# Performance work log

Hardware: AMD Instinct MI355X
Metric: run time of the kernel (lower is better)

Reference implementation:

```python
import jax, jax.numpy as jnp
import numpy as np
from jax import lax

K = 20
EPS = 1e-5
SLOPE = 0.2


def knn_idx(x, k):
    # x: [B, C, N] -> idx [B, N, k] of nearest neighbors (incl. self)
    inner = jnp.einsum('bcn,bcm->bnm', x, x)
    sq = jnp.sum(x * x, axis=1)                      # [B, N]
    neg_d = -(sq[:, :, None] + sq[:, None, :] - 2.0 * inner)
    _, idx = lax.top_k(neg_d, k)
    return idx


def graph_feature(x, idx):
    # x: [B, C, N], idx: [B, N, k] -> [B, 2C, N, k]
    B = x.shape[0]
    xt = jnp.transpose(x, (0, 2, 1))                 # [B, N, C]
    neigh = xt[jnp.arange(B)[:, None, None], idx]    # [B, N, k, C]
    center = jnp.broadcast_to(xt[:, :, None, :], neigh.shape)
    feat = jnp.concatenate([neigh - center, center], axis=-1)  # [B, N, k, 2C]
    return jnp.transpose(feat, (0, 3, 1, 2))         # [B, 2C, N, k]


def conv_bn_lrelu(feat, W, gamma, beta):
    # 1x1 Conv2d (no bias) + eval-mode BN (mean=0, var=1) + LeakyReLU(0.2)
    y = jnp.einsum('oc,bcnk->bonk', W, feat)
    scale = gamma / jnp.sqrt(1.0 + EPS)
    y = y * scale[None, :, None, None] + beta[None, :, None, None]
    return jnp.where(y >= 0, y, SLOPE * y)


def setup_inputs() -> dict:
    key = jax.random.key(0)
    ks = jax.random.split(key, 16)
    B, N, emb = 4, 2048, 1024
    d = {'x': jax.random.normal(ks[0], (B, 3, N), dtype=jnp.float32)}
    dims = [(64, 6), (64, 128), (128, 128), (256, 256), (emb, 256)]
    for i, (o, c) in enumerate(dims):
        d[f'W{i+1}'] = jax.random.normal(ks[1 + i], (o, c), dtype=jnp.float32) * (1.0 / np.sqrt(c))
        d[f'g{i+1}'] = 1.0 + 0.1 * jax.random.normal(ks[6 + i], (o,), dtype=jnp.float32)
        d[f'b{i+1}'] = 0.1 * jax.random.normal(ks[11 + i], (o,), dtype=jnp.float32)
    return d


def reference(x, W1, W2, W3, W4, W5, g1, g2, g3, g4, g5, b1, b2, b3, b4, b5):
    # EdgeConv block 1
    f = graph_feature(x, knn_idx(x, K))              # [B, 6, N, k]
    x1 = jnp.max(conv_bn_lrelu(f, W1, g1, b1), axis=-1)   # [B, 64, N]
    # EdgeConv block 2
    f = graph_feature(x1, knn_idx(x1, K))            # [B, 128, N, k]
    x2 = jnp.max(conv_bn_lrelu(f, W2, g2, b2), axis=-1)   # [B, 64, N]
    # EdgeConv block 3
    f = graph_feature(x2, knn_idx(x2, K))            # [B, 128, N, k]
    x3 = jnp.max(conv_bn_lrelu(f, W3, g3, b3), axis=-1)   # [B, 128, N]
    # EdgeConv block 4
    f = graph_feature(x3, knn_idx(x3, K))            # [B, 256, N, k]
    x4 = jnp.max(conv_bn_lrelu(f, W4, g4, b4), axis=-1)   # [B, 256, N]
    # conv5 (1x1 over points) + global max pool
    x5 = conv_bn_lrelu(x4[:, :, :, None], W5, g5, b5)     # [B, emb, N, 1]
    return jnp.max(x5[..., 0], axis=-1)              # [B, emb]
```

## Files before the change

### kernel.cpp

```cpp
#include <hip/hip_runtime.h>
#include <math.h>

#define BB 4
#define NN 2048
#define KK 20
#define INFPK 0xFFFFFFFFFFFFFFFFull

static __device__ __forceinline__ float lrelu(float z) {
    return z >= 0.f ? z : 0.2f * z;
}

template<int CTRL>
static __device__ __forceinline__ unsigned long long dpp_min64_step(unsigned long long v) {
    unsigned lo = (unsigned)__builtin_amdgcn_update_dpp(
        (int)0xFFFFFFFFu, (int)(unsigned)v, CTRL, 0xF, 0xF, false);
    unsigned hi = (unsigned)__builtin_amdgcn_update_dpp(
        (int)0xFFFFFFFFu, (int)(unsigned)(v >> 32), CTRL, 0xF, 0xF, false);
    unsigned long long t = ((unsigned long long)hi << 32) | lo;
    return t < v ? t : v;
}
static __device__ __forceinline__ unsigned long long wave_min64_bcast(unsigned long long v) {
    v = dpp_min64_step<0x111>(v);
    v = dpp_min64_step<0x112>(v);
    v = dpp_min64_step<0x114>(v);
    v = dpp_min64_step<0x118>(v);
    v = dpp_min64_step<0x142>(v);
    v = dpp_min64_step<0x143>(v);
    unsigned lo = (unsigned)__builtin_amdgcn_readlane((int)(unsigned)v, 63);
    unsigned hi = (unsigned)__builtin_amdgcn_readlane((int)(unsigned)(v >> 32), 63);
    return ((unsigned long long)hi << 32) | lo;
}

template<int C>
__global__ __launch_bounds__(256) void sq_kernel(const float* __restrict__ x,
                                                 float* __restrict__ sq) {
    int i = blockIdx.x * 256 + threadIdx.x;
    if (i >= BB * NN) return;
    int b = i / NN, n = i - b * NN;
    const float* xb = x + (size_t)b * C * NN + n;
    float s = 0.f;
    #pragma unroll
    for (int c = 0; c < C; ++c) {
        float v = xb[(size_t)c * NN];
        s = fmaf(v, v, s);
    }
    sq[i] = s;
}

template<int C>
__global__ __launch_bounds__(512) void knn_kernel(const float* __restrict__ x,
                                                  const float* __restrict__ sq,
                                                  int* __restrict__ idx) {
    const int QT = 8;
    __shared__ unsigned dl[QT][NN];
    __shared__ float xq[QT][C];
    __shared__ float sqq[QT];
    int blk = blockIdx.x;
    int b = blk / (NN / QT);
    int q0 = (blk - b * (NN / QT)) * QT;
    int t = threadIdx.x;
    int lane = t & 63, wid = t >> 6;

    const float* xb = x + (size_t)b * C * NN;
    for (int e = t; e < QT * C; e += 512) {
        int q = e / C, c = e - q * C;
        xq[q][c] = xb[(size_t)c * NN + q0 + q];
    }
    if (t < QT) sqq[t] = sq[b * NN + q0 + t];
    __syncthreads();

    float acc[QT][4];
    #pragma unroll
    for (int q = 0; q < QT; ++q)
        #pragma unroll
        for (int u = 0; u < 4; ++u) acc[q][u] = 0.f;

    for (int c = 0; c < C; ++c) {
        float4 xj = *(const float4*)&xb[(size_t)c * NN + 4 * t];
        #pragma unroll
        for (int q = 0; q < QT; ++q) {
            float xqc = xq[q][c];
            acc[q][0] = fmaf(xqc, xj.x, acc[q][0]);
            acc[q][1] = fmaf(xqc, xj.y, acc[q][1]);
            acc[q][2] = fmaf(xqc, xj.z, acc[q][2]);
            acc[q][3] = fmaf(xqc, xj.w, acc[q][3]);
        }
    }
    float4 sqj = *(const float4*)&sq[b * NN + 4 * t];
    float sqju[4] = {sqj.x, sqj.y, sqj.z, sqj.w};

    int wbase = ((t >> 3) << 5) | (((t ^ (t >> 3)) & 7) << 2);
    #pragma unroll
    for (int q = 0; q < QT; ++q) {
        float sqi = sqq[q];
        uint4 kv;
        unsigned ks[4];
        #pragma unroll
        for (int u = 0; u < 4; ++u) {
            float d = sqi + sqju[u] - 2.f * acc[q][u];
            unsigned v = __float_as_uint(d);
            ks[u] = v ^ ((unsigned)((int)v >> 31) | 0x80000000u);
        }
        kv.x = ks[0]; kv.y = ks[1]; kv.z = ks[2]; kv.w = ks[3];
        *(uint4*)&dl[q][wbase] = kv;
    }
    __syncthreads();

    unsigned* dq = &dl[wid][0];
    int r7 = lane & 7;
    int lanebase = lane << 5;

    unsigned long long h0 = INFPK, h1 = INFPK, h2 = INFPK, h3 = INFPK;

#define PK_INS(KEY, LO) {                                                     \
        unsigned long long v =                                                \
            ((unsigned long long)(KEY) << 12) | (unsigned)(lanebase + (LO));  \
        if (v < h3) {                                                         \
            unsigned long long nh3 = h2 > v ? h2 : v;                         \
            unsigned long long t2  = h2 < v ? h2 : v;                         \
            unsigned long long nh2 = h1 > t2 ? h1 : t2;                       \
            unsigned long long t1  = h1 < v ? h1 : v;                         \
            unsigned long long nh1 = h0 > t1 ? h0 : t1;                       \
            unsigned long long nh0 = h0 < v ? h0 : v;                         \
            h0 = nh0; h1 = nh1; h2 = nh2; h3 = nh3;                           \
        } }
#define PK_INS_THR(KEY, LO) {                                                 \
        unsigned long long v =                                                \
            ((unsigned long long)(KEY) << 12) | (unsigned)(lanebase + (LO));  \
        if (v > thr && v < h3) {                                              \
            unsigned long long nh3 = h2 > v ? h2 : v;                         \
            unsigned long long t2  = h2 < v ? h2 : v;                         \
            unsigned long long nh2 = h1 > t2 ? h1 : t2;                       \
            unsigned long long t1  = h1 < v ? h1 : v;                         \
            unsigned long long nh1 = h0 > t1 ? h0 : t1;                       \
            unsigned long long nh0 = h0 < v ? h0 : v;                         \
            h0 = nh0; h1 = nh1; h2 = nh2; h3 = nh3;                           \
        } }
#define CHUNK_RD(c) uint4 V##c = *(const uint4*)(dq + lanebase + (((c) ^ r7) << 2));
#define CHUNK_INS(c)     { PK_INS(V##c.x, 4*(c)+0) PK_INS(V##c.y, 4*(c)+1)        \
                           PK_INS(V##c.z, 4*(c)+2) PK_INS(V##c.w, 4*(c)+3) }
#define CHUNK_INS_THR(c) { PK_INS_THR(V##c.x, 4*(c)+0) PK_INS_THR(V##c.y, 4*(c)+1) \
                           PK_INS_THR(V##c.z, 4*(c)+2) PK_INS_THR(V##c.w, 4*(c)+3) }

    {
        CHUNK_RD(0) CHUNK_RD(1) CHUNK_RD(2) CHUNK_RD(3)
        CHUNK_RD(4) CHUNK_RD(5) CHUNK_RD(6) CHUNK_RD(7)
        CHUNK_INS(0) CHUNK_INS(1) CHUNK_INS(2) CHUNK_INS(3)
        CHUNK_INS(4) CHUNK_INS(5) CHUNK_INS(6) CHUNK_INS(7)
    }

    int* orow = idx + (size_t)(b * NN + q0 + wid) * KK;
    unsigned long long thr = 0;
    int popped = 0;
    #pragma unroll 1
    for (int rr = 0; rr < KK; ++rr) {
        unsigned long long g = wave_min64_bcast(h0);
        if (lane == 0) orow[rr] = (int)(g & 0xFFFu);
        if (h0 == g) {
            thr = g;
            ++popped;
            h0 = h1; h1 = h2; h2 = h3; h3 = INFPK;
            if (h0 == INFPK && popped < 32) {
                CHUNK_RD(0) CHUNK_RD(1) CHUNK_RD(2) CHUNK_RD(3)
                CHUNK_RD(4) CHUNK_RD(5) CHUNK_RD(6) CHUNK_RD(7)
                CHUNK_INS_THR(0) CHUNK_INS_THR(1) CHUNK_INS_THR(2) CHUNK_INS_THR(3)
                CHUNK_INS_THR(4) CHUNK_INS_THR(5) CHUNK_INS_THR(6) CHUNK_INS_THR(7)
            }
        }
    }
#undef PK_INS
#undef PK_INS_THR
#undef CHUNK_RD
#undef CHUNK_INS
#undef CHUNK_INS_THR
}

template<int C, int OT>
__global__ __launch_bounds__(256) void pt_kernel(const float* __restrict__ x,
                                                 const float* __restrict__ W,
                                                 float* __restrict__ p,
                                                 float* __restrict__ tt,
                                                 int O) {
    const int NB = NN / 256;
    int blk = blockIdx.x;
    int nb = blk % NB;
    int rest = blk / NB;
    int nob = O / OT;
    int ob = rest % nob;
    int b = rest / nob;
    int t = threadIdx.x;
    int n = nb * 256 + t;
    __shared__ float wn[OT][C], wd[OT][C];
    for (int e = t; e < OT * C; e += 256) {
        int o = e / C, c = e - o * C;
        float a = W[(size_t)(ob * OT + o) * (2 * C) + c];
        float b2 = W[(size_t)(ob * OT + o) * (2 * C) + C + c];
        wn[o][c] = a;
        wd[o][c] = b2 - a;
    }
    __syncthreads();
    float ap[OT], at[OT];
    #pragma unroll
    for (int o = 0; o < OT; ++o) { ap[o] = 0.f; at[o] = 0.f; }
    const float* xb = x + (size_t)b * C * NN + n;
    for (int c = 0; c < C; ++c) {
        float xv = xb[(size_t)c * NN];
        #pragma unroll
        for (int o = 0; o < OT; ++o) {
            ap[o] = fmaf(wn[o][c], xv, ap[o]);
            at[o] = fmaf(wd[o][c], xv, at[o]);
        }
    }
    size_t base = ((size_t)b * O + ob * OT) * NN + n;
    #pragma unroll
    for (int o = 0; o < OT; ++o) {
        p[base + (size_t)o * NN] = ap[o];
        tt[base + (size_t)o * NN] = at[o];
    }
}

__global__ __launch_bounds__(256) void edge_kernel(const float* __restrict__ p,
                                                   const float* __restrict__ tt,
                                                   const int* __restrict__ idx,
                                                   const float* __restrict__ g,
                                                   const float* __restrict__ be,
                                                   float* __restrict__ out, int O) {
    int b = blockIdx.x / O, o = blockIdx.x - b * O;
    __shared__ float pl[NN];
    const float* pr = p + ((size_t)b * O + o) * NN;
    for (int e = threadIdx.x * 4; e < NN; e += 1024)
        *(float4*)&pl[e] = *(const float4*)&pr[e];
    __syncthreads();
    float scale = g[o] / sqrtf(1.f + 1e-5f);
    float beta = be[o];
    const float* tr = tt + ((size_t)b * O + o) * NN;
    float* orow = out + ((size_t)b * O + o) * NN;
    for (int i = threadIdx.x; i < NN; i += 256) {
        float ti = tr[i];
        const int4* ir4 = (const int4*)(idx + (size_t)(b * NN + i) * KK);
        int4 w0 = ir4[0], w1 = ir4[1], w2 = ir4[2], w3 = ir4[3], w4 = ir4[4];
        float m = -__builtin_inff();
        int js[20] = {w0.x, w0.y, w0.z, w0.w, w1.x, w1.y, w1.z, w1.w,
                      w2.x, w2.y, w2.z, w2.w, w3.x, w3.y, w3.z, w3.w,
                      w4.x, w4.y, w4.z, w4.w};
        #pragma unroll
        for (int k = 0; k < KK; ++k) {
            float y = pl[js[k]] + ti;
            m = fmaxf(m, lrelu(fmaf(scale, y, beta)));
        }
        orow[i] = m;
    }
}

__global__ __launch_bounds__(256) void transpose_kernel(const float* __restrict__ W,
                                                        float* __restrict__ WT) {
    __shared__ float tile[32][33];
    int c0 = blockIdx.x * 32, o0 = blockIdx.y * 32;
    int tx = threadIdx.x, ty = threadIdx.y;
    #pragma unroll
    for (int i = 0; i < 32; i += 8)
        tile[ty + i][tx] = W[(size_t)(o0 + ty + i) * 256 + c0 + tx];
    __syncthreads();
    #pragma unroll
    for (int i = 0; i < 32; i += 8)
        WT[(size_t)(c0 + ty + i) * 1024 + o0 + tx] = tile[tx][ty + i];
}

__global__ __launch_bounds__(256) void final_kernel(const float* __restrict__ x4,
                                                    const float* __restrict__ W5T,
                                                    const float* __restrict__ g,
                                                    const float* __restrict__ be,
                                                    float* __restrict__ partial) {
    const int CC = 256;
    __shared__ float xs[64][64];
    __shared__ float ws[64][64];
    int blk = blockIdx.x;
    int nb = blk & 31;
    int ob = (blk >> 5) & 15;
    int b  = blk >> 9;
    int t = threadIdx.x;
    int tn = t & 15, to = t >> 4;

    float acc[4][4];
    #pragma unroll
    for (int i = 0; i < 4; ++i)
        #pragma unroll
        for (int j = 0; j < 4; ++j) acc[i][j] = 0.f;

    for (int c0 = 0; c0 < CC; c0 += 64) {
        __syncthreads();
        #pragma unroll
        for (int e = t * 4; e < 64 * 64; e += 1024) {
            int c = e >> 6, n = e & 63;
            *(float4*)&xs[c][n] =
                *(const float4*)&x4[((size_t)b * CC + c0 + c) * NN + nb * 64 + n];
        }
        #pragma unroll
        for (int e = t * 4; e < 64 * 64; e += 1024) {
            int c = e >> 6, o = e & 63;
            *(float4*)&ws[c][o] =
                *(const float4*)&W5T[(size_t)(c0 + c) * 1024 + ob * 64 + o];
        }
        __syncthreads();
        for (int c = 0; c < 64; ++c) {
            float4 xv = *(float4*)&xs[c][tn * 4];
            float4 wv = *(float4*)&ws[c][to * 4];
            acc[0][0] = fmaf(wv.x, xv.x, acc[0][0]);
            acc[0][1] = fmaf(wv.x, xv.y, acc[0][1]);
            acc[0][2] = fmaf(wv.x, xv.z, acc[0][2]);
            acc[0][3] = fmaf(wv.x, xv.w, acc[0][3]);
            acc[1][0] = fmaf(wv.y, xv.x, acc[1][0]);
            acc[1][1] = fmaf(wv.y, xv.y, acc[1][1]);
            acc[1][2] = fmaf(wv.y, xv.z, acc[1][2]);
            acc[1][3] = fmaf(wv.y, xv.w, acc[1][3]);
            acc[2][0] = fmaf(wv.z, xv.x, acc[2][0]);
            acc[2][1] = fmaf(wv.z, xv.y, acc[2][1]);
            acc[2][2] = fmaf(wv.z, xv.z, acc[2][2]);
            acc[2][3] = fmaf(wv.z, xv.w, acc[2][3]);
            acc[3][0] = fmaf(wv.w, xv.x, acc[3][0]);
            acc[3][1] = fmaf(wv.w, xv.y, acc[3][1]);
            acc[3][2] = fmaf(wv.w, xv.z, acc[3][2]);
            acc[3][3] = fmaf(wv.w, xv.w, acc[3][3]);
        }
    }

    float rs = 1.f / sqrtf(1.f + 1e-5f);
    #pragma unroll
    for (int i = 0; i < 4; ++i) {
        int o = ob * 64 + to * 4 + i;
        float scale = g[o] * rs, beta = be[o];
        float m = -__builtin_inff();
        #pragma unroll
        for (int j = 0; j < 4; ++j)
            m = fmaxf(m, lrelu(fmaf(scale, acc[i][j], beta)));
        #pragma unroll
        for (int off = 8; off >= 1; off >>= 1)
            m = fmaxf(m, __shfl_xor(m, off));
        if (tn == 0)
            partial[(size_t)(nb * BB + b) * 1024 + o] = m;
    }
}

__global__ __launch_bounds__(256) void reduce32_kernel(const float* __restrict__ partial,
                                                       float* __restrict__ out) {
    int i = blockIdx.x * 256 + threadIdx.x;
    if (i >= BB * 1024) return;
    int b = i >> 10, o = i & 1023;
    float m = -__builtin_inff();
    #pragma unroll
    for (int nb = 0; nb < 32; ++nb)
        m = fmaxf(m, partial[(size_t)(nb * BB + b) * 1024 + o]);
    out[i] = m;
}

extern "C" void kernel_launch(void* const* d_in, const int* in_sizes, int n_in,
                              void* d_out, int out_size, void* d_ws, size_t ws_size,
                              hipStream_t stream) {
    const float* x  = (const float*)d_in[0];
    const float* W1 = (const float*)d_in[1];
    const float* g1 = (const float*)d_in[2];
    const float* b1 = (const float*)d_in[3];
    const float* W2 = (const float*)d_in[4];
    const float* g2 = (const float*)d_in[5];
    const float* b2 = (const float*)d_in[6];
    const float* W3 = (const float*)d_in[7];
    const float* g3 = (const float*)d_in[8];
    const float* b3 = (const float*)d_in[9];
    const float* W4 = (const float*)d_in[10];
    const float* g4 = (const float*)d_in[11];
    const float* b4 = (const float*)d_in[12];
    const float* W5 = (const float*)d_in[13];
    const float* g5 = (const float*)d_in[14];
    const float* b5 = (const float*)d_in[15];

    float* ws = (float*)d_ws;
    float* sq      = ws;
    int*   idx     = (int*)(ws + 8192);
    float* x1      = ws + 8192 + 163840;
    float* x2      = x1 + 524288;
    float* x3      = x2 + 524288;
    float* x4      = x3 + 1048576;
    float* p       = x4 + 2097152;
    float* tt      = p + 2097152;
    float* W5T     = p;
    float* partial = tt;

    dim3 blk(256), kblk(512);

    sq_kernel<3><<<32, blk, 0, stream>>>(x, sq);
    knn_kernel<3><<<BB * (NN / 8), kblk, 0, stream>>>(x, sq, idx);
    pt_kernel<3, 16><<<BB * (64 / 16) * (NN / 256), blk, 0, stream>>>(x, W1, p, tt, 64);
    edge_kernel<<<BB * 64, blk, 0, stream>>>(p, tt, idx, g1, b1, x1, 64);

    sq_kernel<64><<<32, blk, 0, stream>>>(x1, sq);
    knn_kernel<64><<<BB * (NN / 8), kblk, 0, stream>>>(x1, sq, idx);
    pt_kernel<64, 16><<<BB * (64 / 16) * (NN / 256), blk, 0, stream>>>(x1, W2, p, tt, 64);
    edge_kernel<<<BB * 64, blk, 0, stream>>>(p, tt, idx, g2, b2, x2, 64);

    sq_kernel<64><<<32, blk, 0, stream>>>(x2, sq);
    knn_kernel<64><<<BB * (NN / 8), kblk, 0, stream>>>(x2, sq, idx);
    pt_kernel<64, 16><<<BB * (128 / 16) * (NN / 256), blk, 0, stream>>>(x2, W3, p, tt, 128);
    edge_kernel<<<BB * 128, blk, 0, stream>>>(p, tt, idx, g3, b3, x3, 128);

    sq_kernel<128><<<32, blk, 0, stream>>>(x3, sq);
    knn_kernel<128><<<BB * (NN / 8), kblk, 0, stream>>>(x3, sq, idx);
    pt_kernel<128, 16><<<BB * (256 / 16) * (NN / 256), blk, 0, stream>>>(x3, W4, p, tt, 256);
    edge_kernel<<<BB * 256, blk, 0, stream>>>(p, tt, idx, g4, b4, x4, 256);

    transpose_kernel<<<dim3(8, 32), dim3(32, 8), 0, stream>>>(W5, W5T);
    final_kernel<<<BB * 16 * 32, blk, 0, stream>>>(x4, W5T, g5, b5, partial);
    reduce32_kernel<<<16, blk, 0, stream>>>(partial, (float*)d_out);
}
```

Measured before the change: 562.1 us.

## Split KNN into tiled distance GEMM and per-row top-k selection kernels

When the workspace is large enough, KNN becomes two kernels. A tiled 64x64 distance kernel computes the full distance key matrix (4x2048x2048 unsigned) with shared-memory reuse, and a separate wave-per-row selection kernel finds the top 20. This replaces the fused knn_kernel, which restreamed all candidate points from global memory for every group of 8 queries. The fallback knn_kernel now computes the squared norms inline instead of reading them from sq_kernel. The split path writes and reads about 64MB of keys per block, trading extra memory traffic for better compute reuse.

```diff
diff --git a/kernel.cpp b/kernel.cpp
--- a/kernel.cpp
+++ b/kernel.cpp
@@ -48,8 +48,156 @@
 }
 
 template<int C>
+__global__ __launch_bounds__(256, 4) void dist_kernel(const float* __restrict__ x,
+                                                      const float* __restrict__ sq,
+                                                      unsigned* __restrict__ keys) {
+    __shared__ float xi[64][64];
+    __shared__ float xj[64][64];
+    int blk = blockIdx.x;
+    int jt = blk & 31;
+    int it = (blk >> 5) & 31;
+    int b  = blk >> 10;
+    int t = threadIdx.x;
+    int tn = t & 15, to = t >> 4;
+
+    float acc[4][4];
+    #pragma unroll
+    for (int i = 0; i < 4; ++i)
+        #pragma unroll
+        for (int j = 0; j < 4; ++j) acc[i][j] = 0.f;
+
+    const float* xb = x + (size_t)b * C * NN;
+    for (int c0 = 0; c0 < C; c0 += 64) {
+        const int CT = (C - c0) < 64 ? (C - c0) : 64;
+        __syncthreads();
+        for (int e = t * 4; e < CT * 64; e += 1024) {
+            int c = e >> 6, i = e & 63;
+            *(float4*)&xi[c][i] = *(const float4*)&xb[(size_t)(c0 + c) * NN + it * 64 + i];
+        }
+        for (int e = t * 4; e < CT * 64; e += 1024) {
+            int c = e >> 6, j = e & 63;
+            *(float4*)&xj[c][j] = *(const float4*)&xb[(size_t)(c0 + c) * NN + jt * 64 + j];
+        }
+        __syncthreads();
+        for (int c = 0; c < CT; ++c) {
+            float4 iv = *(float4*)&xi[c][to * 4];
+            float4 jv = *(float4*)&xj[c][tn * 4];
+            acc[0][0] = fmaf(iv.x, jv.x, acc[0][0]);
+            acc[0][1] = fmaf(iv.x, jv.y, acc[0][1]);
+            acc[0][2] = fmaf(iv.x, jv.z, acc[0][2]);
+            acc[0][3] = fmaf(iv.x, jv.w, acc[0][3]);
+            acc[1][0] = fmaf(iv.y, jv.x, acc[1][0]);
+            acc[1][1] = fmaf(iv.y, jv.y, acc[1][1]);
+            acc[1][2] = fmaf(iv.y, jv.z, acc[1][2]);
+            acc[1][3] = fmaf(iv.y, jv.w, acc[1][3]);
+            acc[2][0] = fmaf(iv.z, jv.x, acc[2][0]);
+            acc[2][1] = fmaf(iv.z, jv.y, acc[2][1]);
+            acc[2][2] = fmaf(iv.z, jv.z, acc[2][2]);
+            acc[2][3] = fmaf(iv.z, jv.w, acc[2][3]);
+            acc[3][0] = fmaf(iv.w, jv.x, acc[3][0]);
+            acc[3][1] = fmaf(iv.w, jv.y, acc[3][1]);
+            acc[3][2] = fmaf(iv.w, jv.z, acc[3][2]);
+            acc[3][3] = fmaf(iv.w, jv.w, acc[3][3]);
+        }
+    }
+
+    const float* sqb = sq + b * NN;
+    float4 sqjv = *(const float4*)&sqb[jt * 64 + tn * 4];
+    float sqju[4] = {sqjv.x, sqjv.y, sqjv.z, sqjv.w};
+    #pragma unroll
+    for (int i = 0; i < 4; ++i) {
+        float sqi = sqb[it * 64 + to * 4 + i];
+        uint4 kv;
+        unsigned ks[4];
+        #pragma unroll
+        for (int u = 0; u < 4; ++u) {
+            float d = sqi + sqju[u] - 2.f * acc[i][u];
+            unsigned v = __float_as_uint(d);
+            ks[u] = v ^ ((unsigned)((int)v >> 31) | 0x80000000u);
+        }
+        kv.x = ks[0]; kv.y = ks[1]; kv.z = ks[2]; kv.w = ks[3];
+        *(uint4*)&keys[((size_t)b * NN + it * 64 + to * 4 + i) * NN + jt * 64 + tn * 4] = kv;
+    }
+}
+
+__global__ __launch_bounds__(256) void select_kernel(const unsigned* __restrict__ keys,
+                                                     int* __restrict__ idx) {
+    int t = threadIdx.x;
+    int lane = t & 63, wid = t >> 6;
+    int Q = blockIdx.x * 4 + wid;
+    const unsigned* row = keys + (size_t)Q * NN;
+
+    unsigned long long h0 = INFPK, h1 = INFPK, h2 = INFPK, h3 = INFPK;
+
+#define PK_INS(KEY, J) {                                                      \
+        unsigned long long v =                                                \
+            ((unsigned long long)(KEY) << 12) | (unsigned)(J);                \
+        if (v < h3) {                                                         \
+            unsigned long long nh3 = h2 > v ? h2 : v;                         \
+            unsigned long long t2  = h2 < v ? h2 : v;                         \
+            unsigned long long nh2 = h1 > t2 ? h1 : t2;                       \
+            unsigned long long t1  = h1 < v ? h1 : v;                         \
+            unsigned long long nh1 = h0 > t1 ? h0 : t1;                       \
+            unsigned long long nh0 = h0 < v ? h0 : v;                         \
+            h0 = nh0; h1 = nh1; h2 = nh2; h3 = nh3;                           \
+        } }
+#define PK_INS_THR(KEY, J) {                                                  \
+        unsigned long long v =                                                \
+            ((unsigned long long)(KEY) << 12) | (unsigned)(J);                \
+        if (v > thr && v < h3) {                                              \
+            unsigned long long nh3 = h2 > v ? h2 : v;                         \
+            unsigned long long t2  = h2 < v ? h2 : v;                         \
+            unsigned long long nh2 = h1 > t2 ? h1 : t2;                       \
+            unsigned long long t1  = h1 < v ? h1 : v;                         \
+            unsigned long long nh1 = h0 > t1 ? h0 : t1;                       \
+            unsigned long long nh0 = h0 < v ? h0 : v;                         \
+            h0 = nh0; h1 = nh1; h2 = nh2; h3 = nh3;                           \
+        } }
+#define ROW_RD(s) uint4 V##s = *(const uint4*)(row + 4 * (lane + 64 * (s)));
+#define ROW_INS(s)     { PK_INS(V##s.x, 4*lane + 256*(s) + 0)                 \
+                         PK_INS(V##s.y, 4*lane + 256*(s) + 1)                 \
+                         PK_INS(V##s.z, 4*lane + 256*(s) + 2)                 \
+                         PK_INS(V##s.w, 4*lane + 256*(s) + 3) }
+#define ROW_INS_THR(s) { PK_INS_THR(V##s.x, 4*lane + 256*(s) + 0)             \
+                         PK_INS_THR(V##s.y, 4*lane + 256*(s) + 1)             \
+                         PK_INS_THR(V##s.z, 4*lane + 256*(s) + 2)             \
+                         PK_INS_THR(V##s.w, 4*lane + 256*(s) + 3) }
+
+    {
+        ROW_RD(0) ROW_RD(1) ROW_RD(2) ROW_RD(3)
+        ROW_RD(4) ROW_RD(5) ROW_RD(6) ROW_RD(7)
+        ROW_INS(0) ROW_INS(1) ROW_INS(2) ROW_INS(3)
+        ROW_INS(4) ROW_INS(5) ROW_INS(6) ROW_INS(7)
+    }
+
+    int* orow = idx + (size_t)Q * KK;
+    unsigned long long thr = 0;
+    int popped = 0;
+    #pragma unroll 1
+    for (int rr = 0; rr < KK; ++rr) {
+        unsigned long long g = wave_min64_bcast(h0);
+        if (lane == 0) orow[rr] = (int)(g & 0xFFFu);
+        if (h0 == g) {
+            thr = g;
+            ++popped;
+            h0 = h1; h1 = h2; h2 = h3; h3 = INFPK;
+            if (h0 == INFPK && popped < 32) {
+                ROW_RD(0) ROW_RD(1) ROW_RD(2) ROW_RD(3)
+                ROW_RD(4) ROW_RD(5) ROW_RD(6) ROW_RD(7)
+                ROW_INS_THR(0) ROW_INS_THR(1) ROW_INS_THR(2) ROW_INS_THR(3)
+                ROW_INS_THR(4) ROW_INS_THR(5) ROW_INS_THR(6) ROW_INS_THR(7)
+            }
+        }
+    }
+#undef PK_INS
+#undef PK_INS_THR
+#undef ROW_RD
+#undef ROW_INS
+#undef ROW_INS_THR
+}
+
+template<int C>
 __global__ __launch_bounds__(512) void knn_kernel(const float* __restrict__ x,
-                                                  const float* __restrict__ sq,
                                                   int* __restrict__ idx) {
     const int QT = 8;
     __shared__ unsigned dl[QT][NN];
@@ -66,28 +214,38 @@
         int q = e / C, c = e - q * C;
         xq[q][c] = xb[(size_t)c * NN + q0 + q];
     }
-    if (t < QT) sqq[t] = sq[b * NN + q0 + t];
     __syncthreads();
+    if (t < QT) {
+        float s = 0.f;
+        #pragma unroll 4
+        for (int c = 0; c < C; ++c) s = fmaf(xq[t][c], xq[t][c], s);
+        sqq[t] = s;
+    }
+    __syncthreads();
 
     float acc[QT][4];
     #pragma unroll
     for (int q = 0; q < QT; ++q)
         #pragma unroll
         for (int u = 0; u < 4; ++u) acc[q][u] = 0.f;
+    float sqa0 = 0.f, sqa1 = 0.f, sqa2 = 0.f, sqa3 = 0.f;
 
     for (int c = 0; c < C; ++c) {
-        float4 xj = *(const float4*)&xb[(size_t)c * NN + 4 * t];
+        float4 xjv = *(const float4*)&xb[(size_t)c * NN + 4 * t];
         #pragma unroll
         for (int q = 0; q < QT; ++q) {
             float xqc = xq[q][c];
-            acc[q][0] = fmaf(xqc, xj.x, acc[q][0]);
-            acc[q][1] = fmaf(xqc, xj.y, acc[q][1]);
-            acc[q][2] = fmaf(xqc, xj.z, acc[q][2]);
-            acc[q][3] = fmaf(xqc, xj.w, acc[q][3]);
-        }
-    }
-    float4 sqj = *(const float4*)&sq[b * NN + 4 * t];
-    float sqju[4] = {sqj.x, sqj.y, sqj.z, sqj.w};
+            acc[q][0] = fmaf(xqc, xjv.x, acc[q][0]);
+            acc[q][1] = fmaf(xqc, xjv.y, acc[q][1]);
+            acc[q][2] = fmaf(xqc, xjv.z, acc[q][2]);
+            acc[q][3] = fmaf(xqc, xjv.w, acc[q][3]);
+        }
+        sqa0 = fmaf(xjv.x, xjv.x, sqa0);
+        sqa1 = fmaf(xjv.y, xjv.y, sqa1);
+        sqa2 = fmaf(xjv.z, xjv.z, sqa2);
+        sqa3 = fmaf(xjv.w, xjv.w, sqa3);
+    }
+    float sqju[4] = {sqa0, sqa1, sqa2, sqa3};
 
     int wbase = ((t >> 3) << 5) | (((t ^ (t >> 3)) & 7) << 2);
     #pragma unroll
@@ -109,7 +267,6 @@
     unsigned* dq = &dl[wid][0];
     int r7 = lane & 7;
     int lanebase = lane << 5;
-
     unsigned long long h0 = INFPK, h1 = INFPK, h2 = INFPK, h3 = INFPK;
 
 #define PK_INS(KEY, LO) {                                                     \
@@ -374,38 +531,66 @@
     const float* b5 = (const float*)d_in[15];
 
     float* ws = (float*)d_ws;
-    float* sq      = ws;
-    int*   idx     = (int*)(ws + 8192);
-    float* x1      = ws + 8192 + 163840;
-    float* x2      = x1 + 524288;
-    float* x3      = x2 + 524288;
-    float* x4      = x3 + 1048576;
-    float* p       = x4 + 2097152;
-    float* tt      = p + 2097152;
-    float* W5T     = p;
-    float* partial = tt;
+    float*   sqv = ws;
+    int*     idx = (int*)(ws + 8192);
+    float*   x1  = ws + 8192 + 163840;
+    float*   x2  = x1 + 524288;
+    float*   x3  = x2 + 524288;
+    float*   x4  = x3 + 1048576;
+    float*   big = x4 + 2097152;
+    float*   p   = big;
+    float*   tt  = p + 2097152;
+    unsigned* keys = (unsigned*)big;
+    float*   W5T     = p;
+    float*   partial = tt;
+
+    const size_t need_new = (size_t)(8192 + 163840 + 524288 + 524288 + 1048576
+                                     + 2097152 + 16777216) * 4;
+    const bool use_split = ws_size >= need_new;
 
     dim3 blk(256), kblk(512);
 
-    sq_kernel<3><<<32, blk, 0, stream>>>(x, sq);
-    knn_kernel<3><<<BB * (NN / 8), kblk, 0, stream>>>(x, sq, idx);
-    pt_kernel<3, 16><<<BB * (64 / 16) * (NN / 256), blk, 0, stream>>>(x, W1, p, tt, 64);
-    edge_kernel<<<BB * 64, blk, 0, stream>>>(p, tt, idx, g1, b1, x1, 64);
-
-    sq_kernel<64><<<32, blk, 0, stream>>>(x1, sq);
-    knn_kernel<64><<<BB * (NN / 8), kblk, 0, stream>>>(x1, sq, idx);
-    pt_kernel<64, 16><<<BB * (64 / 16) * (NN / 256), blk, 0, stream>>>(x1, W2, p, tt, 64);
-    edge_kernel<<<BB * 64, blk, 0, stream>>>(p, tt, idx, g2, b2, x2, 64);
-
-    sq_kernel<64><<<32, blk, 0, stream>>>(x2, sq);
-    knn_kernel<64><<<BB * (NN / 8), kblk, 0, stream>>>(x2, sq, idx);
-    pt_kernel<64, 16><<<BB * (128 / 16) * (NN / 256), blk, 0, stream>>>(x2, W3, p, tt, 128);
-    edge_kernel<<<BB * 128, blk, 0, stream>>>(p, tt, idx, g3, b3, x3, 128);
-
-    sq_kernel<128><<<32, blk, 0, stream>>>(x3, sq);
-    knn_kernel<128><<<BB * (NN / 8), kblk, 0, stream>>>(x3, sq, idx);
-    pt_kernel<128, 16><<<BB * (256 / 16) * (NN / 256), blk, 0, stream>>>(x3, W4, p, tt, 256);
-    edge_kernel<<<BB * 256, blk, 0, stream>>>(p, tt, idx, g4, b4, x4, 256);
+    if (use_split) {
+        sq_kernel<3><<<32, blk, 0, stream>>>(x, sqv);
+        dist_kernel<3><<<BB * 32 * 32, blk, 0, stream>>>(x, sqv, keys);
+        select_kernel<<<BB * NN / 4, blk, 0, stream>>>(keys, idx);
+        pt_kernel<3, 16><<<BB * 4 * 8, blk, 0, stream>>>(x, W1, p, tt, 64);
+        edge_kernel<<<BB * 64, blk, 0, stream>>>(p, tt, idx, g1, b1, x1, 64);
+
+        sq_kernel<64><<<32, blk, 0, stream>>>(x1, sqv);
+        dist_kernel<64><<<BB * 32 * 32, blk, 0, stream>>>(x1, sqv, keys);
+        select_kernel<<<BB * NN / 4, blk, 0, stream>>>(keys, idx);
+        pt_kernel<64, 16><<<BB * 4 * 8, blk, 0, stream>>>(x1, W2, p, tt, 64);
+        edge_kernel<<<BB * 64, blk, 0, stream>>>(p, tt, idx, g2, b2, x2, 64);
+
+        sq_kernel<64><<<32, blk, 0, stream>>>(x2, sqv);
+        dist_kernel<64><<<BB * 32 * 32, blk, 0, stream>>>(x2, sqv, keys);
+        select_kernel<<<BB * NN / 4, blk, 0, stream>>>(keys, idx);
+        pt_kernel<64, 16><<<BB * 8 * 8, blk, 0, stream>>>(x2, W3, p, tt, 128);
+        edge_kernel<<<BB * 128, blk, 0, stream>>>(p, tt, idx, g3, b3, x3, 128);
+
+        sq_kernel<128><<<32, blk, 0, stream>>>(x3, sqv);
+        dist_kernel<128><<<BB * 32 * 32, blk, 0, stream>>>(x3, sqv, keys);
+        select_kernel<<<BB * NN / 4, blk, 0, stream>>>(keys, idx);
+        pt_kernel<128, 16><<<BB * 16 * 8, blk, 0, stream>>>(x3, W4, p, tt, 256);
+        edge_kernel<<<BB * 256, blk, 0, stream>>>(p, tt, idx, g4, b4, x4, 256);
+    } else {
+        knn_kernel<3><<<BB * (NN / 8), kblk, 0, stream>>>(x, idx);
+        pt_kernel<3, 16><<<BB * 4 * 8, blk, 0, stream>>>(x, W1, p, tt, 64);
+        edge_kernel<<<BB * 64, blk, 0, stream>>>(p, tt, idx, g1, b1, x1, 64);
+
+        knn_kernel<64><<<BB * (NN / 8), kblk, 0, stream>>>(x1, idx);
+        pt_kernel<64, 16><<<BB * 4 * 8, blk, 0, stream>>>(x1, W2, p, tt, 64);
+        edge_kernel<<<BB * 64, blk, 0, stream>>>(p, tt, idx, g2, b2, x2, 64);
+
+        knn_kernel<64><<<BB * (NN / 8), kblk, 0, stream>>>(x2, idx);
+        pt_kernel<64, 16><<<BB * 8 * 8, blk, 0, stream>>>(x2, W3, p, tt, 128);
+        edge_kernel<<<BB * 128, blk, 0, stream>>>(p, tt, idx, g3, b3, x3, 128);
+
+        knn_kernel<128><<<BB * (NN / 8), kblk, 0, stream>>>(x3, idx);
+        pt_kernel<128, 16><<<BB * 16 * 8, blk, 0, stream>>>(x3, W4, p, tt, 256);
+        edge_kernel<<<BB * 256, blk, 0, stream>>>(p, tt, idx, g4, b4, x4, 256);
+    }
 
     transpose_kernel<<<dim3(8, 32), dim3(32, 8), 0, stream>>>(W5, W5T);
     final_kernel<<<BB * 16 * 32, blk, 0, stream>>>(x4, W5T, g5, b5, partial);
```

Result: slower. 602.0 us (+7.1%).
